# Kernel optimization log

Measured on AMD Instinct MI355X. Metric: run time of the kernel, lower is better.

Reference implementation:

```python
import jax, jax.numpy as jnp
import numpy as np

B, L, D = 2, 256, 256  # batch, length, raw feature dim (W dims are D+1)

def setup_inputs() -> dict:
    key = jax.random.key(0)
    k1, k2, k3, kw = jax.random.split(key, 4)
    layer1 = jax.random.normal(k1, (B, L, D), dtype=jnp.float32)
    layer2 = jax.random.normal(k2, (B, L, D), dtype=jnp.float32)
    layer3 = jax.random.normal(k3, (B, L, D), dtype=jnp.float32)
    # xavier_normal_ for a 3D tensor: fan_in = D+1 * (D+1) receptive? torch treats
    # dim0 as fan_out-ish; we just use a matched-scale gaussian (correctness of the
    # contraction math is what matters for the kernel baseline).
    std = float(np.sqrt(2.0 / ((D + 1) + (D + 1) * (D + 1))))
    W = jax.random.normal(kw, (D + 1, D + 1, D + 1), dtype=jnp.float32) * std
    return {"layer1": layer1, "layer2": layer2, "layer3": layer3, "W": W}

def _append_ones(x):
    ones = jnp.ones(x.shape[:2] + (1,), dtype=x.dtype)
    return jnp.concatenate([x, ones], axis=-1)

def reference(layer1, layer2, layer3, W):
    l1 = _append_ones(layer1)  # [n, L, a]
    l2 = _append_ones(layer2)  # [n, L, b]
    l3 = _append_ones(layer3)  # [n, L, c]
    # Chained contraction: nia,abc -> nibc ; nibc,njb -> nijc ; nijc,nkc -> nijk
    t = jnp.einsum('nia,abc->nibc', l1, W)
    t = jnp.einsum('nibc,njb->nijc', t, l2)
    out = jnp.einsum('nijc,nkc->nijk', t, l3)
    return out
```

## Files before the change

kernel.cpp:

```cpp
#include <hip/hip_runtime.h>

typedef unsigned short u16;
typedef __attribute__((ext_vector_type(8))) short bf16x8;
typedef __attribute__((ext_vector_type(4))) float f32x4;

#define GLOAD_LDS16(gsrc, ldst)                                               \
  __builtin_amdgcn_global_load_lds(                                           \
      (const __attribute__((address_space(1))) void*)(gsrc),                  \
      (__attribute__((address_space(3))) void*)(ldst), 16, 0, 0)

#define LDSOFF(p) \
  ((unsigned)(uintptr_t)(__attribute__((address_space(3))) const void*)(p))

#define SB0 __builtin_amdgcn_sched_barrier(0)

__device__ __forceinline__ u16 f2bf(float x) {
  unsigned u = __float_as_uint(x);
  u = (u + 0x7FFFu + ((u >> 16) & 1u)) >> 16;
  return (u16)u;
}

__global__ void prep_l_kernel(const float* __restrict__ l1,
                              const float* __restrict__ l2,
                              const float* __restrict__ l3,
                              u16* __restrict__ o1, u16* __restrict__ o2,
                              u16* __restrict__ o3) {
  int idx = blockIdx.x * 256 + threadIdx.x;
  const int NR = 512 * 288;
  if (idx >= 3 * NR) return;
  int which = idx / NR, rem = idx - which * NR;
  int r = rem / 288, p = rem - r * 288;
  const float* s = which == 0 ? l1 : which == 1 ? l2 : l3;
  u16* d = which == 0 ? o1 : which == 1 ? o2 : o3;
  float v = (p < 256) ? s[r * 256 + p] : (p == 256 ? 1.0f : 0.0f);
  d[rem] = f2bf(v);
}

__global__ __launch_bounds__(256, 4) void prep_w_kernel(
    const float* __restrict__ W, u16* __restrict__ W2) {
  __shared__ float tf[64][65];
  const int a0 = blockIdx.x * 64, c0 = blockIdx.y * 64, b = blockIdx.z;
  const int t = threadIdx.x;
  const bool bok = (b < 257);

  float v[16];
#pragma unroll
  for (int i = 0; i < 16; ++i) {
    int idx = t + i * 256;
    int ar = idx >> 6, cc = idx & 63;
    int a = a0 + ar, c = c0 + cc;
    v[i] = (bok && a < 257 && c < 257) ? W[((long)a * 257 + b) * 257 + c] : 0.0f;
  }
#pragma unroll
  for (int i = 0; i < 16; ++i) {
    int idx = t + i * 256;
    int ar = idx >> 6, cc = idx & 63;
    tf[cc][ar] = v[i];
  }
  __syncthreads();

#pragma unroll
  for (int p = 0; p < 2; ++p) {
    int q = t + p * 256;
    int cr = q >> 3, ach = q & 7;
    int c = c0 + cr;
    int abase = a0 + ach * 8;
    if (c < 288 && abase < 288) {
      u16 pk[8];
#pragma unroll
      for (int j = 0; j < 8; ++j) pk[j] = f2bf(tf[cr][ach * 8 + j]);
      *(uint4*)(&W2[((long)c * 288 + b) * 288 + abase]) = *(uint4*)pk;
    }
  }
}

__global__ __launch_bounds__(256, 3) void gemm_nt(
    const u16* __restrict__ A, const u16* __restrict__ B, u16* __restrict__ C,
    int K, int lda, int ldb, int ldc) {
  __shared__ u16 As[2][4096];
  __shared__ u16 Bs[2][4096];
  const int t = threadIdx.x;
  const int bid = blockIdx.x;
  const int xcd = bid & 7, s = bid >> 3;
  const int nt = xcd * 81 + (s >> 2);
  const int mt = s & 3;
  const int m0 = mt * 128, n0 = nt * 128;
  const int lane = t & 63;
  const int w = t >> 6;
  const int wr = (w >> 1) * 64, wc = (w & 1) * 64;
  const int r16 = lane & 15;
  const int cgrp = lane >> 4;
  const int rr = cgrp * 4;
  const unsigned ABase = LDSOFF(&As[0][0]);
  const unsigned BBase = LDSOFF(&Bs[0][0]);
  (void)K;

  const u16* PA = A + (long)m0 * lda;
  const u16* PB = B + (long)n0 * ldb;

#define STG(buf, k0)                                                          \
  {                                                                           \
    _Pragma("unroll") for (int _p = 0; _p < 2; ++_p) {                        \
      int _q = t + _p * 256;                                                  \
      int _r = _q >> 2, _g = (_q & 3) ^ ((_r >> 1) & 3);                      \
      GLOAD_LDS16(PA + (long)_r * lda + (k0) + _g * 8, &As[buf][_q * 8]);     \
      GLOAD_LDS16(PB + (long)_r * ldb + (k0) + _g * 8, &Bs[buf][_q * 8]);     \
    }                                                                         \
  }

  f32x4 acc[4][4];
  const f32x4 zero = {0.f, 0.f, 0.f, 0.f};
#pragma unroll
  for (int i = 0; i < 4; ++i)
#pragma unroll
    for (int j = 0; j < 4; ++j) acc[i][j] = zero;

  STG(0, 0);

#define GCOL(NI)                                                              \
  __builtin_amdgcn_s_setprio(1);                                              \
  _Pragma("unroll") for (int _mi = 0; _mi < 4; ++_mi)                         \
    acc[_mi][NI] = __builtin_amdgcn_mfma_f32_16x16x32_bf16(                   \
        af[_mi], bf[NI], acc[_mi][NI], 0, 0, 0);                              \
  __builtin_amdgcn_s_setprio(0);                                              \
  SB0;

#define GSTEP(KS)                                                             \
  {                                                                           \
    asm volatile("s_waitcnt vmcnt(0)" ::: "memory");                          \
    SB0;                                                                      \
    __builtin_amdgcn_s_barrier();                                             \
    SB0;                                                                      \
    bf16x8 af[4], bf[4];                                                      \
    _Pragma("unroll") for (int mi = 0; mi < 4; ++mi) {                        \
      int R = wr + mi * 16 + r16;                                             \
      unsigned ao = ABase + (unsigned)(((((KS) & 1) * 4096) + R * 32 +        \
                                       ((cgrp ^ ((R >> 1) & 3)) * 8)) * 2);   \
      asm volatile("ds_read_b128 %0, %1" : "=v"(af[mi]) : "v"(ao));           \
    }                                                                         \
    _Pragma("unroll") for (int ni = 0; ni < 4; ++ni) {                        \
      int R = wc + ni * 16 + r16;                                             \
      unsigned ao = BBase + (unsigned)(((((KS) & 1) * 4096) + R * 32 +        \
                                       ((cgrp ^ ((R >> 1) & 3)) * 8)) * 2);   \
      asm volatile("ds_read_b128 %0, %1" : "=v"(bf[ni]) : "v"(ao));           \
    }                                                                         \
    SB0;                                                                      \
    if ((KS) < 8) STG(((KS) + 1) & 1, ((KS) + 1) * 32);                       \
    SB0;                                                                      \
    asm volatile("s_waitcnt lgkmcnt(3)" ::: "memory"); SB0;                   \
    GCOL(0)                                                                   \
    asm volatile("s_waitcnt lgkmcnt(2)" ::: "memory"); SB0;                   \
    GCOL(1)                                                                   \
    asm volatile("s_waitcnt lgkmcnt(1)" ::: "memory"); SB0;                   \
    GCOL(2)                                                                   \
    asm volatile("s_waitcnt lgkmcnt(0)" ::: "memory"); SB0;                   \
    GCOL(3)                                                                   \
  }

  GSTEP(0) GSTEP(1) GSTEP(2) GSTEP(3) GSTEP(4)
  GSTEP(5) GSTEP(6) GSTEP(7) GSTEP(8)
#undef GSTEP
#undef GCOL
#undef STG

#pragma unroll
  for (int mi = 0; mi < 4; ++mi) {
    int gm = m0 + wr + mi * 16 + rr;
#pragma unroll
    for (int ni = 0; ni < 4; ++ni) {
      int gc = n0 + wc + ni * 16 + r16;
#pragma unroll
      for (int r = 0; r < 4; ++r)
        C[(long)(gm + r) * ldc + gc] = f2bf(acc[mi][ni][r]);
    }
  }
}

__global__ __launch_bounds__(512, 4) void fused23(
    const u16* __restrict__ l2b, const u16* __restrict__ l3b,
    const u16* __restrict__ T1, float* __restrict__ out) {
  __shared__ u16 S[64 * 296];
  __shared__ u16 Bst[2][288 * 32];
  const int t = threadIdx.x;
  const int lane = t & 63;
  const int w = t >> 6;

  const int bid = blockIdx.x;
  const int xcd = bid & 7;
  const int seq = bid >> 3;
  const int ni = xcd * 64 + (seq >> 2);
  const int q = seq & 3;
  const int n = ni >> 8;

  const int r16 = lane & 15;
  const int cgrp = lane >> 4;
  const int kb = cgrp * 8;
  const int rr = cgrp * 4;
  const f32x4 zero = {0.f, 0.f, 0.f, 0.f};

  const u16* A2 = l2b + (long)n * 73728 + (long)(q * 64) * 288;
  const u16* BT = T1 + (long)ni * 82944;
  const u16* B3 = l3b + (long)n * 73728;
  const unsigned BOF = LDSOFF(&Bst[0][0]);
  const unsigned SOF = LDSOFF(&S[0]);

#define ISSUE_A(buf, kk)                                                      \
  {                                                                           \
    _Pragma("unroll") for (int _p = 0; _p < 3; ++_p) {                        \
      int _q = t + _p * 512;                                                  \
      if (_q < 1152) {                                                        \
        int _r = _q >> 2, _g = (_q & 3) ^ ((_r >> 1) & 3);                    \
        GLOAD_LDS16(BT + (long)_r * 288 + (kk) * 32 + _g * 8,                 \
                    &Bst[(buf)][_q * 8]);                                     \
      }                                                                       \
    }                                                                         \
  }
#define ISSUE_B(buf, kk)                                                      \
  {                                                                           \
    _Pragma("unroll") for (int _p = 0; _p < 2; ++_p) {                        \
      int _q = t + _p * 512;                                                  \
      int _r = _q >> 2, _g = (_q & 3) ^ ((_r >> 1) & 3);                      \
      GLOAD_LDS16(B3 + (long)_r * 288 + (kk) * 32 + _g * 8,                   \
                  &Bst[(buf)][_q * 8]);                                       \
    }                                                                         \
  }

  {
    const int wj = w & 3, wc2 = w >> 2;
    const u16* Ap = A2 + (long)(wj * 16 + r16) * 288 + kb;
    f32x4 acc[9];
#pragma unroll
    for (int j = 0; j < 9; ++j) acc[j] = zero;

    ISSUE_A(0, 0);
    bf16x8 afrA = *(const bf16x8*)(Ap);
    bf16x8 afrB;
    SB0;

#define FA_MM(NJ, AFC)                                                        \
  __builtin_amdgcn_s_setprio(1);                                              \
  acc[NJ] = __builtin_amdgcn_mfma_f32_16x16x32_bf16(AFC, bf[NJ], acc[NJ], 0, 0, 0); \
  __builtin_amdgcn_s_setprio(0);

#define FA_STEP(K, AFC, AFN)                                                  \
  {                                                                           \
    asm volatile("s_waitcnt vmcnt(0)" ::: "memory");                          \
    SB0;                                                                      \
    __builtin_amdgcn_s_barrier();                                             \
    SB0;                                                                      \
    if ((K) < 8) {                                                            \
      ISSUE_A(((K) + 1) & 1, (K) + 1);                                        \
      AFN = *(const bf16x8*)(Ap + ((K) + 1) * 32);                            \
    }                                                                         \
    SB0;                                                                      \
    bf16x8 bf[9];                                                             \
    _Pragma("unroll") for (int nj = 0; nj < 9; ++nj) {                        \
      const int R = wc2 * 144 + nj * 16 + r16;                                \
      unsigned ao = BOF + (unsigned)((((K) & 1) * 9216 + R * 32 +             \
                                      ((cgrp ^ ((R >> 1) & 3)) * 8)) * 2);    \
      asm volatile("ds_read_b128 %0, %1" : "=v"(bf[nj]) : "v"(ao));           \
    }                                                                         \
    SB0;                                                                      \
    asm volatile("s_waitcnt lgkmcnt(6)" ::: "memory"); SB0;                   \
    FA_MM(0, AFC) FA_MM(1, AFC) FA_MM(2, AFC) SB0;                            \
    asm volatile("s_waitcnt lgkmcnt(3)" ::: "memory"); SB0;                   \
    FA_MM(3, AFC) FA_MM(4, AFC) FA_MM(5, AFC) SB0;                            \
    asm volatile("s_waitcnt lgkmcnt(0)" ::: "memory"); SB0;                   \
    FA_MM(6, AFC) FA_MM(7, AFC) FA_MM(8, AFC) SB0;                            \
  }
    FA_STEP(0, afrA, afrB) FA_STEP(1, afrB, afrA)
    FA_STEP(2, afrA, afrB) FA_STEP(3, afrB, afrA)
    FA_STEP(4, afrA, afrB) FA_STEP(5, afrB, afrA)
    FA_STEP(6, afrA, afrB) FA_STEP(7, afrB, afrA)
    FA_STEP(8, afrA, afrB)
#undef FA_STEP
#undef FA_MM

    __syncthreads();
    ISSUE_B(0, 0);
#pragma unroll
    for (int nj = 0; nj < 9; ++nj)
#pragma unroll
      for (int qq = 0; qq < 4; ++qq)
        S[(wj * 16 + rr + qq) * 296 + wc2 * 144 + nj * 16 + r16] =
            f2bf(acc[nj][qq]);
  }
  __syncthreads();

  {
    const int wjb = w & 1, wk = w >> 1;
    f32x4 acc[2][4];
#pragma unroll
    for (int i = 0; i < 2; ++i)
#pragma unroll
      for (int j = 0; j < 4; ++j) acc[i][j] = zero;

#define FB_MM(NI)                                                             \
  __builtin_amdgcn_s_setprio(1);                                              \
  acc[0][NI] = __builtin_amdgcn_mfma_f32_16x16x32_bf16(af[0], bf[NI], acc[0][NI], 0, 0, 0); \
  acc[1][NI] = __builtin_amdgcn_mfma_f32_16x16x32_bf16(af[1], bf[NI], acc[1][NI], 0, 0, 0); \
  __builtin_amdgcn_s_setprio(0);                                              \
  SB0;

#define FB_STEP(K)                                                            \
  {                                                                           \
    asm volatile("s_waitcnt vmcnt(0)" ::: "memory");                          \
    SB0;                                                                      \
    __builtin_amdgcn_s_barrier();                                             \
    SB0;                                                                      \
    if ((K) < 8) ISSUE_B(((K) + 1) & 1, (K) + 1);                             \
    SB0;                                                                      \
    bf16x8 af[2], bf[4];                                                      \
    _Pragma("unroll") for (int mi = 0; mi < 2; ++mi) {                        \
      unsigned ao = SOF + (unsigned)(((wjb * 32 + mi * 16 + r16) * 296 +      \
                                      (K) * 32 + kb) * 2);                    \
      asm volatile("ds_read_b128 %0, %1" : "=v"(af[mi]) : "v"(ao));           \
    }                                                                         \
    _Pragma("unroll") for (int nj = 0; nj < 4; ++nj) {                        \
      const int R = wk * 64 + nj * 16 + r16;                                  \
      unsigned ao = BOF + (unsigned)((((K) & 1) * 9216 + R * 32 +             \
                                      ((cgrp ^ ((R >> 1) & 3)) * 8)) * 2);    \
      asm volatile("ds_read_b128 %0, %1" : "=v"(bf[nj]) : "v"(ao));           \
    }                                                                         \
    SB0;                                                                      \
    asm volatile("s_waitcnt lgkmcnt(3)" ::: "memory"); SB0;                   \
    FB_MM(0)                                                                  \
    asm volatile("s_waitcnt lgkmcnt(2)" ::: "memory"); SB0;                   \
    FB_MM(1)                                                                  \
    asm volatile("s_waitcnt lgkmcnt(1)" ::: "memory"); SB0;                   \
    FB_MM(2)                                                                  \
    asm volatile("s_waitcnt lgkmcnt(0)" ::: "memory"); SB0;                   \
    FB_MM(3)                                                                  \
  }
    FB_STEP(0) FB_STEP(1) FB_STEP(2) FB_STEP(3) FB_STEP(4)
    FB_STEP(5) FB_STEP(6) FB_STEP(7) FB_STEP(8)
#undef FB_STEP
#undef FB_MM

    float* O = out + (long)ni * 65536 + (long)(q * 64 + wjb * 32) * 256 + wk * 64;
#pragma unroll
    for (int mi = 0; mi < 2; ++mi)
#pragma unroll
      for (int nj = 0; nj < 4; ++nj)
#pragma unroll
        for (int qq = 0; qq < 4; ++qq)
          O[(long)(mi * 16 + rr + qq) * 256 + nj * 16 + r16] = acc[mi][nj][qq];
  }
#undef ISSUE_A
#undef ISSUE_B
}

extern "C" void kernel_launch(void* const* d_in, const int* in_sizes, int n_in,
                              void* d_out, int out_size, void* d_ws, size_t ws_size,
                              hipStream_t stream) {
  const float* l1 = (const float*)d_in[0];
  const float* l2 = (const float*)d_in[1];
  const float* l3 = (const float*)d_in[2];
  const float* W = (const float*)d_in[3];
  float* out = (float*)d_out;
  char* ws = (char*)d_ws;

  const long LB = 512L * 288 * 2;
  u16* l1b = (u16*)ws;
  u16* l2b = (u16*)(ws + LB);
  u16* l3b = (u16*)(ws + 2 * LB);
  u16* T1 = (u16*)(ws + 3 * LB);
  u16* W2 = (u16*)d_out;

  prep_l_kernel<<<1728, 256, 0, stream>>>(l1, l2, l3, l1b, l2b, l3b);

  dim3 gw(5, 5, 288);
  prep_w_kernel<<<gw, 256, 0, stream>>>(W, W2);

  gemm_nt<<<2592, 256, 0, stream>>>(l1b, W2, T1, 288, 288, 288, 82944);

  fused23<<<2048, 512, 0, stream>>>(l2b, l3b, T1, out);
}
```

Measured before the change: 146.3 us.

## Deepen fused23 LDS prefetch pipeline and overlap phase-B loads with phase A

Reworks the fused23 kernel's load schedule. Global-to-LDS copies now run two stages ahead with partial vmcnt waits instead of draining to zero each step. All nine A fragments are preloaded into registers up front. Phase-B tiles of l3 are split into half-k chunks with a new swizzled layout and start loading during the last phase-A steps, which removes the full __syncthreads between phases. This costs an extra barrier per step and more register pressure from keeping the A fragments resident.

```diff
diff --git a/kernel.cpp b/kernel.cpp
--- a/kernel.cpp
+++ b/kernel.cpp
@@ -180,7 +180,7 @@
     const u16* __restrict__ l2b, const u16* __restrict__ l3b,
     const u16* __restrict__ T1, float* __restrict__ out) {
   __shared__ u16 S[64 * 296];
-  __shared__ u16 Bst[2][288 * 32];
+  __shared__ u16 Bst[2][9216];
   const int t = threadIdx.x;
   const int lane = t & 63;
   const int w = t >> 6;
@@ -203,55 +203,53 @@
   const u16* B3 = l3b + (long)n * 73728;
   const unsigned BOF = LDSOFF(&Bst[0][0]);
   const unsigned SOF = LDSOFF(&S[0]);
+  char* BstB = (char*)&Bst[0][0];
 
 #define ISSUE_A(buf, kk)                                                      \
   {                                                                           \
-    _Pragma("unroll") for (int _p = 0; _p < 3; ++_p) {                        \
-      int _q = t + _p * 512;                                                  \
-      if (_q < 1152) {                                                        \
-        int _r = _q >> 2, _g = (_q & 3) ^ ((_r >> 1) & 3);                    \
-        GLOAD_LDS16(BT + (long)_r * 288 + (kk) * 32 + _g * 8,                 \
-                    &Bst[(buf)][_q * 8]);                                     \
-      }                                                                       \
-    }                                                                         \
-  }
-#define ISSUE_B(buf, kk)                                                      \
-  {                                                                           \
-    _Pragma("unroll") for (int _p = 0; _p < 2; ++_p) {                        \
-      int _q = t + _p * 512;                                                  \
-      int _r = _q >> 2, _g = (_q & 3) ^ ((_r >> 1) & 3);                      \
-      GLOAD_LDS16(B3 + (long)_r * 288 + (kk) * 32 + _g * 8,                   \
-                  &Bst[(buf)][_q * 8]);                                       \
-    }                                                                         \
+    int _q1 = w * 144 + lane;                                                 \
+    int _r1 = _q1 >> 2, _g1 = (_q1 & 3) ^ ((_r1 >> 1) & 3);                   \
+    GLOAD_LDS16(BT + (long)_r1 * 288 + (kk) * 32 + _g1 * 8,                   \
+                &Bst[(buf)][_q1 * 8]);                                        \
+    int _q2 = _q1 + 64;                                                       \
+    int _r2 = _q2 >> 2, _g2 = (_q2 & 3) ^ ((_r2 >> 1) & 3);                   \
+    GLOAD_LDS16(BT + (long)_r2 * 288 + (kk) * 32 + _g2 * 8,                   \
+                &Bst[(buf)][_q2 * 8]);                                        \
+    if (lane < 16) {                                                          \
+      int _q3 = w * 144 + 128 + lane;                                         \
+      int _r3 = _q3 >> 2, _g3 = (_q3 & 3) ^ ((_r3 >> 1) & 3);                 \
+      GLOAD_LDS16(BT + (long)_r3 * 288 + (kk) * 32 + _g3 * 8,                 \
+                  &Bst[(buf)][_q3 * 8]);                                      \
+    }                                                                         \
+  }
+#define ISSUE_BH(h)                                                           \
+  {                                                                           \
+    int _q1 = w * 64 + lane;                                                  \
+    int _r1 = _q1 >> 1, _g1 = (_q1 & 1) ^ ((_r1 >> 2) & 1);                   \
+    GLOAD_LDS16(B3 + (long)_r1 * 288 + (h) * 16 + _g1 * 8,                    \
+                BstB + ((((((h) >> 1) & 1) ? 0 : 18432) +                     \
+                         ((h) & 1) * 8192 + _q1 * 16)));                      \
   }
 
   {
     const int wj = w & 3, wc2 = w >> 2;
-    const u16* Ap = A2 + (long)(wj * 16 + r16) * 288 + kb;
     f32x4 acc[9];
 #pragma unroll
     for (int j = 0; j < 9; ++j) acc[j] = zero;
 
-    ISSUE_A(0, 0);
-    bf16x8 afrA = *(const bf16x8*)(Ap);
-    bf16x8 afrB;
+    bf16x8 afr[9];
+#pragma unroll
+    for (int k = 0; k < 9; ++k)
+      afr[k] = *(const bf16x8*)(A2 + (long)(wj * 16 + r16) * 288 + k * 32 + kb);
     SB0;
-
-#define FA_MM(NJ, AFC)                                                        \
-  __builtin_amdgcn_s_setprio(1);                                              \
-  acc[NJ] = __builtin_amdgcn_mfma_f32_16x16x32_bf16(AFC, bf[NJ], acc[NJ], 0, 0, 0); \
-  __builtin_amdgcn_s_setprio(0);
-
-#define FA_STEP(K, AFC, AFN)                                                  \
-  {                                                                           \
-    asm volatile("s_waitcnt vmcnt(0)" ::: "memory");                          \
-    SB0;                                                                      \
-    __builtin_amdgcn_s_barrier();                                             \
-    SB0;                                                                      \
-    if ((K) < 8) {                                                            \
-      ISSUE_A(((K) + 1) & 1, (K) + 1);                                        \
-      AFN = *(const bf16x8*)(Ap + ((K) + 1) * 32);                            \
-    }                                                                         \
+    ISSUE_A(0, 0) SB0;
+    ISSUE_A(1, 1) SB0;
+
+#define FA_STEP(K, NW, ISS)                                                   \
+  {                                                                           \
+    asm volatile("s_waitcnt vmcnt(" #NW ")" ::: "memory");                    \
+    SB0;                                                                      \
+    __builtin_amdgcn_s_barrier();                                             \
     SB0;                                                                      \
     bf16x8 bf[9];                                                             \
     _Pragma("unroll") for (int nj = 0; nj < 9; ++nj) {                        \
@@ -260,24 +258,30 @@
                                       ((cgrp ^ ((R >> 1) & 3)) * 8)) * 2);    \
       asm volatile("ds_read_b128 %0, %1" : "=v"(bf[nj]) : "v"(ao));           \
     }                                                                         \
-    SB0;                                                                      \
-    asm volatile("s_waitcnt lgkmcnt(6)" ::: "memory"); SB0;                   \
-    FA_MM(0, AFC) FA_MM(1, AFC) FA_MM(2, AFC) SB0;                            \
-    asm volatile("s_waitcnt lgkmcnt(3)" ::: "memory"); SB0;                   \
-    FA_MM(3, AFC) FA_MM(4, AFC) FA_MM(5, AFC) SB0;                            \
-    asm volatile("s_waitcnt lgkmcnt(0)" ::: "memory"); SB0;                   \
-    FA_MM(6, AFC) FA_MM(7, AFC) FA_MM(8, AFC) SB0;                            \
-  }
-    FA_STEP(0, afrA, afrB) FA_STEP(1, afrB, afrA)
-    FA_STEP(2, afrA, afrB) FA_STEP(3, afrB, afrA)
-    FA_STEP(4, afrA, afrB) FA_STEP(5, afrB, afrA)
-    FA_STEP(6, afrA, afrB) FA_STEP(7, afrB, afrA)
-    FA_STEP(8, afrA, afrB)
+    asm volatile("s_waitcnt lgkmcnt(0)" ::: "memory");                        \
+    SB0;                                                                      \
+    __builtin_amdgcn_s_barrier();                                             \
+    SB0;                                                                      \
+    ISS                                                                       \
+    SB0;                                                                      \
+    __builtin_amdgcn_s_setprio(1);                                            \
+    _Pragma("unroll") for (int nj = 0; nj < 9; ++nj)                          \
+      acc[nj] = __builtin_amdgcn_mfma_f32_16x16x32_bf16(                      \
+          afr[K], bf[nj], acc[nj], 0, 0, 0);                                  \
+    __builtin_amdgcn_s_setprio(0);                                            \
+    SB0;                                                                      \
+  }
+    FA_STEP(0, 3, ISSUE_A(0, 2))
+    FA_STEP(1, 3, ISSUE_A(1, 3))
+    FA_STEP(2, 3, ISSUE_A(0, 4))
+    FA_STEP(3, 3, ISSUE_A(1, 5))
+    FA_STEP(4, 3, ISSUE_A(0, 6))
+    FA_STEP(5, 3, ISSUE_A(1, 7))
+    FA_STEP(6, 3, ISSUE_A(0, 8))
+    FA_STEP(7, 3, ISSUE_BH(0) ISSUE_BH(1))
+    FA_STEP(8, 2, ISSUE_BH(2) ISSUE_BH(3))
 #undef FA_STEP
-#undef FA_MM
-
-    __syncthreads();
-    ISSUE_B(0, 0);
+
 #pragma unroll
     for (int nj = 0; nj < 9; ++nj)
 #pragma unroll
@@ -285,7 +289,10 @@
         S[(wj * 16 + rr + qq) * 296 + wc2 * 144 + nj * 16 + r16] =
             f2bf(acc[nj][qq]);
   }
-  __syncthreads();
+  asm volatile("s_waitcnt lgkmcnt(0)" ::: "memory");
+  SB0;
+  __builtin_amdgcn_s_barrier();
+  SB0;
 
   {
     const int wjb = w & 1, wk = w >> 1;
@@ -295,20 +302,11 @@
 #pragma unroll
       for (int j = 0; j < 4; ++j) acc[i][j] = zero;
 
-#define FB_MM(NI)                                                             \
-  __builtin_amdgcn_s_setprio(1);                                              \
-  acc[0][NI] = __builtin_amdgcn_mfma_f32_16x16x32_bf16(af[0], bf[NI], acc[0][NI], 0, 0, 0); \
-  acc[1][NI] = __builtin_amdgcn_mfma_f32_16x16x32_bf16(af[1], bf[NI], acc[1][NI], 0, 0, 0); \
-  __builtin_amdgcn_s_setprio(0);                                              \
-  SB0;
-
-#define FB_STEP(K)                                                            \
-  {                                                                           \
-    asm volatile("s_waitcnt vmcnt(0)" ::: "memory");                          \
-    SB0;                                                                      \
-    __builtin_amdgcn_s_barrier();                                             \
-    SB0;                                                                      \
-    if ((K) < 8) ISSUE_B(((K) + 1) & 1, (K) + 1);                             \
+#define FB_STEP(K, NW, ISS)                                                   \
+  {                                                                           \
+    asm volatile("s_waitcnt vmcnt(" #NW ")" ::: "memory");                    \
+    SB0;                                                                      \
+    __builtin_amdgcn_s_barrier();                                             \
     SB0;                                                                      \
     bf16x8 af[2], bf[4];                                                      \
     _Pragma("unroll") for (int mi = 0; mi < 2; ++mi) {                        \
@@ -318,24 +316,37 @@
     }                                                                         \
     _Pragma("unroll") for (int nj = 0; nj < 4; ++nj) {                        \
       const int R = wk * 64 + nj * 16 + r16;                                  \
-      unsigned ao = BOF + (unsigned)((((K) & 1) * 9216 + R * 32 +             \
-                                      ((cgrp ^ ((R >> 1) & 3)) * 8)) * 2);    \
+      unsigned ao = BOF + (unsigned)((((K) & 1) ? 0 : 18432) +                \
+                                     (cgrp >> 1) * 8192 + R * 32 +            \
+                                     (((cgrp & 1) ^ ((R >> 2) & 1)) * 16));   \
       asm volatile("ds_read_b128 %0, %1" : "=v"(bf[nj]) : "v"(ao));           \
     }                                                                         \
-    SB0;                                                                      \
-    asm volatile("s_waitcnt lgkmcnt(3)" ::: "memory"); SB0;                   \
-    FB_MM(0)                                                                  \
-    asm volatile("s_waitcnt lgkmcnt(2)" ::: "memory"); SB0;                   \
-    FB_MM(1)                                                                  \
-    asm volatile("s_waitcnt lgkmcnt(1)" ::: "memory"); SB0;                   \
-    FB_MM(2)                                                                  \
-    asm volatile("s_waitcnt lgkmcnt(0)" ::: "memory"); SB0;                   \
-    FB_MM(3)                                                                  \
-  }
-    FB_STEP(0) FB_STEP(1) FB_STEP(2) FB_STEP(3) FB_STEP(4)
-    FB_STEP(5) FB_STEP(6) FB_STEP(7) FB_STEP(8)
+    asm volatile("s_waitcnt lgkmcnt(0)" ::: "memory");                        \
+    SB0;                                                                      \
+    __builtin_amdgcn_s_barrier();                                             \
+    SB0;                                                                      \
+    ISS                                                                       \
+    SB0;                                                                      \
+    __builtin_amdgcn_s_setprio(1);                                            \
+    _Pragma("unroll") for (int nj = 0; nj < 4; ++nj) {                        \
+      acc[0][nj] = __builtin_amdgcn_mfma_f32_16x16x32_bf16(                   \
+          af[0], bf[nj], acc[0][nj], 0, 0, 0);                                \
+      acc[1][nj] = __builtin_amdgcn_mfma_f32_16x16x32_bf16(                   \
+          af[1], bf[nj], acc[1][nj], 0, 0, 0);                                \
+    }                                                                         \
+    __builtin_amdgcn_s_setprio(0);                                            \
+    SB0;                                                                      \
+  }
+    FB_STEP(0, 2, ISSUE_BH(4)  ISSUE_BH(5))
+    FB_STEP(1, 2, ISSUE_BH(6)  ISSUE_BH(7))
+    FB_STEP(2, 2, ISSUE_BH(8)  ISSUE_BH(9))
+    FB_STEP(3, 2, ISSUE_BH(10) ISSUE_BH(11))
+    FB_STEP(4, 2, ISSUE_BH(12) ISSUE_BH(13))
+    FB_STEP(5, 2, ISSUE_BH(14) ISSUE_BH(15))
+    FB_STEP(6, 2, ISSUE_BH(16) ISSUE_BH(17))
+    FB_STEP(7, 2, )
+    FB_STEP(8, 0, )
 #undef FB_STEP
-#undef FB_MM
 
     float* O = out + (long)ni * 65536 + (long)(q * 64 + wjb * 32) * 256 + wk * 64;
 #pragma unroll
@@ -347,7 +358,7 @@
           O[(long)(mi * 16 + rr + qq) * 256 + nj * 16 + r16] = acc[mi][nj][qq];
   }
 #undef ISSUE_A
-#undef ISSUE_B
+#undef ISSUE_BH
 }
 
 extern "C" void kernel_launch(void* const* d_in, const int* in_sizes, int n_in,
```

Result: slower. 172.9 us (+18.2%).

## Trim padded dimensions: exploit ones-column to drop padded tiles and K steps

Applied to the files above, without the earlier changes.

The stage-1 GEMM grid shrinks so fewer N tiles are computed, and the fused kernel now processes only 272 columns (rows up to the ones index) instead of 288 in stage A, with 8 instead of 9 K steps in stage B. The ones-column contribution of layer3 is added as a bias read from the S buffer instead of being multiplied. Stage A warps are remapped to 2x5 tiles with two A fragments per warp. LDS shrinks, and the B prefetch is moved after the fragment reads. There is a risk that truncating the GEMM N range misses needed T1 columns.

```diff
diff --git a/kernel.cpp b/kernel.cpp
--- a/kernel.cpp
+++ b/kernel.cpp
@@ -82,7 +82,7 @@
   const int t = threadIdx.x;
   const int bid = blockIdx.x;
   const int xcd = bid & 7, s = bid >> 3;
-  const int nt = xcd * 81 + (s >> 2);
+  const int nt = xcd * 77 + (s >> 2);
   const int mt = s & 3;
   const int m0 = mt * 128, n0 = nt * 128;
   const int lane = t & 63;
@@ -179,8 +179,8 @@
 __global__ __launch_bounds__(512, 4) void fused23(
     const u16* __restrict__ l2b, const u16* __restrict__ l3b,
     const u16* __restrict__ T1, float* __restrict__ out) {
-  __shared__ u16 S[64 * 296];
-  __shared__ u16 Bst[2][288 * 32];
+  __shared__ u16 S[64 * 280];
+  __shared__ u16 Bst[2][8704];
   const int t = threadIdx.x;
   const int lane = t & 63;
   const int w = t >> 6;
@@ -206,19 +206,25 @@
 
 #define ISSUE_A(buf, kk)                                                      \
   {                                                                           \
-    _Pragma("unroll") for (int _p = 0; _p < 3; ++_p) {                        \
-      int _q = t + _p * 512;                                                  \
-      if (_q < 1152) {                                                        \
-        int _r = _q >> 2, _g = (_q & 3) ^ ((_r >> 1) & 3);                    \
-        GLOAD_LDS16(BT + (long)_r * 288 + (kk) * 32 + _g * 8,                 \
-                    &Bst[(buf)][_q * 8]);                                     \
-      }                                                                       \
+    int _q1 = w * 136 + lane;                                                 \
+    int _r1 = _q1 >> 2, _g1 = (_q1 & 3) ^ ((_r1 >> 1) & 3);                   \
+    GLOAD_LDS16(BT + (long)_r1 * 288 + (kk) * 32 + _g1 * 8,                   \
+                &Bst[(buf)][_q1 * 8]);                                        \
+    int _q2 = _q1 + 64;                                                       \
+    int _r2 = _q2 >> 2, _g2 = (_q2 & 3) ^ ((_r2 >> 1) & 3);                   \
+    GLOAD_LDS16(BT + (long)_r2 * 288 + (kk) * 32 + _g2 * 8,                   \
+                &Bst[(buf)][_q2 * 8]);                                        \
+    if (lane < 8) {                                                           \
+      int _q3 = w * 136 + 128 + lane;                                         \
+      int _r3 = _q3 >> 2, _g3 = (_q3 & 3) ^ ((_r3 >> 1) & 3);                 \
+      GLOAD_LDS16(BT + (long)_r3 * 288 + (kk) * 32 + _g3 * 8,                 \
+                  &Bst[(buf)][_q3 * 8]);                                      \
     }                                                                         \
   }
 #define ISSUE_B(buf, kk)                                                      \
   {                                                                           \
     _Pragma("unroll") for (int _p = 0; _p < 2; ++_p) {                        \
-      int _q = t + _p * 512;                                                  \
+      int _q = w * 128 + lane + _p * 64;                                      \
       int _r = _q >> 2, _g = (_q & 3) ^ ((_r >> 1) & 3);                      \
       GLOAD_LDS16(B3 + (long)_r * 288 + (kk) * 32 + _g * 8,                   \
                   &Bst[(buf)][_q * 8]);                                       \
@@ -226,64 +232,69 @@
   }
 
   {
-    const int wj = w & 3, wc2 = w >> 2;
-    const u16* Ap = A2 + (long)(wj * 16 + r16) * 288 + kb;
-    f32x4 acc[9];
-#pragma unroll
-    for (int j = 0; j < 9; ++j) acc[j] = zero;
-
-    ISSUE_A(0, 0);
-    bf16x8 afrA = *(const bf16x8*)(Ap);
-    bf16x8 afrB;
+    const int wjA = w & 1, wcA = w >> 1;
+    const int NT = (wcA == 3) ? 5 : 4;
+    f32x4 acc[2][5];
+#pragma unroll
+    for (int i = 0; i < 2; ++i)
+#pragma unroll
+      for (int j = 0; j < 5; ++j) acc[i][j] = zero;
+
+    const u16* Ap = A2 + (long)(wjA * 32 + r16) * 288 + kb;
+    bf16x8 afc0 = *(const bf16x8*)(Ap);
+    bf16x8 afc1 = *(const bf16x8*)(Ap + 16 * 288);
+    bf16x8 afn0, afn1;
     SB0;
-
-#define FA_MM(NJ, AFC)                                                        \
-  __builtin_amdgcn_s_setprio(1);                                              \
-  acc[NJ] = __builtin_amdgcn_mfma_f32_16x16x32_bf16(AFC, bf[NJ], acc[NJ], 0, 0, 0); \
-  __builtin_amdgcn_s_setprio(0);
-
-#define FA_STEP(K, AFC, AFN)                                                  \
+    ISSUE_A(0, 0) SB0;
+    ISSUE_A(1, 1) SB0;
+
+#define FA_STEP(K)                                                            \
   {                                                                           \
     asm volatile("s_waitcnt vmcnt(0)" ::: "memory");                          \
     SB0;                                                                      \
     __builtin_amdgcn_s_barrier();                                             \
+    SB0;                                                                      \
+    bf16x8 bf[5];                                                             \
+    _Pragma("unroll") for (int i = 0; i < 5; ++i) if (i < NT) {               \
+      const int R = wcA * 64 + i * 16 + r16;                                  \
+      unsigned ao = BOF + (unsigned)((((K) & 1) * 8704 + R * 32 +             \
+                                      ((cgrp ^ ((R >> 1) & 3)) * 8)) * 2);    \
+      asm volatile("ds_read_b128 %0, %1" : "=v"(bf[i]) : "v"(ao));            \
+    }                                                                         \
     SB0;                                                                      \
     if ((K) < 8) {                                                            \
       ISSUE_A(((K) + 1) & 1, (K) + 1);                                        \
-      AFN = *(const bf16x8*)(Ap + ((K) + 1) * 32);                            \
-    }                                                                         \
-    SB0;                                                                      \
-    bf16x8 bf[9];                                                             \
-    _Pragma("unroll") for (int nj = 0; nj < 9; ++nj) {                        \
-      const int R = wc2 * 144 + nj * 16 + r16;                                \
-      unsigned ao = BOF + (unsigned)((((K) & 1) * 9216 + R * 32 +             \
-                                      ((cgrp ^ ((R >> 1) & 3)) * 8)) * 2);    \
-      asm volatile("ds_read_b128 %0, %1" : "=v"(bf[nj]) : "v"(ao));           \
-    }                                                                         \
-    SB0;                                                                      \
-    asm volatile("s_waitcnt lgkmcnt(6)" ::: "memory"); SB0;                   \
-    FA_MM(0, AFC) FA_MM(1, AFC) FA_MM(2, AFC) SB0;                            \
-    asm volatile("s_waitcnt lgkmcnt(3)" ::: "memory"); SB0;                   \
-    FA_MM(3, AFC) FA_MM(4, AFC) FA_MM(5, AFC) SB0;                            \
-    asm volatile("s_waitcnt lgkmcnt(0)" ::: "memory"); SB0;                   \
-    FA_MM(6, AFC) FA_MM(7, AFC) FA_MM(8, AFC) SB0;                            \
-  }
-    FA_STEP(0, afrA, afrB) FA_STEP(1, afrB, afrA)
-    FA_STEP(2, afrA, afrB) FA_STEP(3, afrB, afrA)
-    FA_STEP(4, afrA, afrB) FA_STEP(5, afrB, afrA)
-    FA_STEP(6, afrA, afrB) FA_STEP(7, afrB, afrA)
-    FA_STEP(8, afrA, afrB)
+      afn0 = *(const bf16x8*)(Ap + ((K) + 1) * 32);                           \
+      afn1 = *(const bf16x8*)(Ap + 16 * 288 + ((K) + 1) * 32);                \
+    }                                                                         \
+    SB0;                                                                      \
+    asm volatile("s_waitcnt lgkmcnt(0)" ::: "memory");                        \
+    SB0;                                                                      \
+    __builtin_amdgcn_s_setprio(1);                                            \
+    _Pragma("unroll") for (int i = 0; i < 5; ++i) if (i < NT) {               \
+      acc[0][i] = __builtin_amdgcn_mfma_f32_16x16x32_bf16(                    \
+          afc0, bf[i], acc[0][i], 0, 0, 0);                                   \
+      acc[1][i] = __builtin_amdgcn_mfma_f32_16x16x32_bf16(                    \
+          afc1, bf[i], acc[1][i], 0, 0, 0);                                   \
+    }                                                                         \
+    __builtin_amdgcn_s_setprio(0);                                            \
+    SB0;                                                                      \
+    afc0 = afn0; afc1 = afn1;                                                 \
+  }
+    FA_STEP(0) FA_STEP(1) FA_STEP(2) FA_STEP(3) FA_STEP(4)
+    FA_STEP(5) FA_STEP(6) FA_STEP(7) FA_STEP(8)
 #undef FA_STEP
-#undef FA_MM
 
     __syncthreads();
     ISSUE_B(0, 0);
 #pragma unroll
-    for (int nj = 0; nj < 9; ++nj)
-#pragma unroll
-      for (int qq = 0; qq < 4; ++qq)
-        S[(wj * 16 + rr + qq) * 296 + wc2 * 144 + nj * 16 + r16] =
-            f2bf(acc[nj][qq]);
+    for (int i = 0; i < 5; ++i) if (i < NT)
+#pragma unroll
+      for (int mi = 0; mi < 2; ++mi)
+#pragma unroll
+        for (int qq = 0; qq < 4; ++qq)
+          S[(wjA * 32 + mi * 16 + rr + qq) * 280 + wcA * 64 + i * 16 + r16] =
+              f2bf(acc[mi][i][qq]);
   }
   __syncthreads();
 
@@ -308,20 +319,20 @@
     SB0;                                                                      \
     __builtin_amdgcn_s_barrier();                                             \
     SB0;                                                                      \
-    if ((K) < 8) ISSUE_B(((K) + 1) & 1, (K) + 1);                             \
-    SB0;                                                                      \
     bf16x8 af[2], bf[4];                                                      \
     _Pragma("unroll") for (int mi = 0; mi < 2; ++mi) {                        \
-      unsigned ao = SOF + (unsigned)(((wjb * 32 + mi * 16 + r16) * 296 +      \
+      unsigned ao = SOF + (unsigned)(((wjb * 32 + mi * 16 + r16) * 280 +      \
                                       (K) * 32 + kb) * 2);                    \
       asm volatile("ds_read_b128 %0, %1" : "=v"(af[mi]) : "v"(ao));           \
     }                                                                         \
     _Pragma("unroll") for (int nj = 0; nj < 4; ++nj) {                        \
       const int R = wk * 64 + nj * 16 + r16;                                  \
-      unsigned ao = BOF + (unsigned)((((K) & 1) * 9216 + R * 32 +             \
+      unsigned ao = BOF + (unsigned)((((K) & 1) * 8704 + R * 32 +             \
                                       ((cgrp ^ ((R >> 1) & 3)) * 8)) * 2);    \
       asm volatile("ds_read_b128 %0, %1" : "=v"(bf[nj]) : "v"(ao));           \
     }                                                                         \
+    SB0;                                                                      \
+    if ((K) < 7) ISSUE_B(((K) + 1) & 1, (K) + 1);                             \
     SB0;                                                                      \
     asm volatile("s_waitcnt lgkmcnt(3)" ::: "memory"); SB0;                   \
     FB_MM(0)                                                                  \
@@ -332,11 +343,19 @@
     asm volatile("s_waitcnt lgkmcnt(0)" ::: "memory"); SB0;                   \
     FB_MM(3)                                                                  \
   }
-    FB_STEP(0) FB_STEP(1) FB_STEP(2) FB_STEP(3) FB_STEP(4)
-    FB_STEP(5) FB_STEP(6) FB_STEP(7) FB_STEP(8)
+    FB_STEP(0) FB_STEP(1) FB_STEP(2) FB_STEP(3)
+    FB_STEP(4) FB_STEP(5) FB_STEP(6) FB_STEP(7)
 #undef FB_STEP
 #undef FB_MM
 
+    float s256[2][4];
+#pragma unroll
+    for (int mi = 0; mi < 2; ++mi)
+#pragma unroll
+      for (int qq = 0; qq < 4; ++qq)
+        s256[mi][qq] = __uint_as_float(
+            (unsigned)S[(wjb * 32 + mi * 16 + rr + qq) * 280 + 256] << 16);
+
     float* O = out + (long)ni * 65536 + (long)(q * 64 + wjb * 32) * 256 + wk * 64;
 #pragma unroll
     for (int mi = 0; mi < 2; ++mi)
@@ -344,7 +363,8 @@
       for (int nj = 0; nj < 4; ++nj)
 #pragma unroll
         for (int qq = 0; qq < 4; ++qq)
-          O[(long)(mi * 16 + rr + qq) * 256 + nj * 16 + r16] = acc[mi][nj][qq];
+          O[(long)(mi * 16 + rr + qq) * 256 + nj * 16 + r16] =
+              acc[mi][nj][qq] + s256[mi][qq];
   }
 #undef ISSUE_A
 #undef ISSUE_B
@@ -372,7 +392,7 @@
   dim3 gw(5, 5, 288);
   prep_w_kernel<<<gw, 256, 0, stream>>>(W, W2);
 
-  gemm_nt<<<2592, 256, 0, stream>>>(l1b, W2, T1, 288, 288, 288, 82944);
+  gemm_nt<<<2464, 256, 0, stream>>>(l1b, W2, T1, 288, 288, 288, 82944);
 
   fused23<<<2048, 512, 0, stream>>>(l2b, l3b, T1, out);
 }
```

New measurement: 147.8 us. Within noise of the previous version (+1.0%).
